# Kernel tuning notes

Measured on AMD Instinct MI355X. Metric: run time of the kernel, lower is better.

## Reference

```python
import jax, jax.numpy as jnp
from jax import lax
import numpy as np

# torch.sign(torch.sign(x) + 0.5): maps x<0 -> -1, x>=0 -> +1 (zeros go to +1)
def binarize(x):
    return jnp.where(x >= 0, 1.0, -1.0).astype(x.dtype)


def setup_inputs() -> dict:
    key = jax.random.key(0)
    kx, kw, kb = jax.random.split(key, 3)
    x = jax.random.normal(kx, (32, 256, 56, 56), dtype=jnp.float32)
    weight = jax.random.normal(kw, (256, 256, 3, 3), dtype=jnp.float32)
    bias = jax.random.normal(kb, (256,), dtype=jnp.float32)
    return {"x": x, "weight": weight, "bias": bias}


def reference(x, weight, bias):
    b_weight = binarize(weight)  # [O, I, kH, kW] in {-1, +1}
    b_bias = binarize(bias)      # [O] in {-1, +1}
    out = lax.conv_general_dilated(
        x, b_weight,
        window_strides=(1, 1),
        padding=((1, 1), (1, 1)),
        rhs_dilation=(1, 1),
        feature_group_count=1,
        dimension_numbers=("NCHW", "OIHW", "NCHW"),
    )
    return out + b_bias[None, :, None, None]
```

## Files before the change

### kernel.cpp

```cpp
#include <hip/hip_runtime.h>
#include <stdint.h>


#define N_IMG 32
#define C_IN  256
#define H_IN  56
#define W_IN  56
#define O_OUT 256
#define HW    (H_IN * W_IN)
#define K_RAW (C_IN * 9)

typedef int8_t i8x16 __attribute__((ext_vector_type(16)));
typedef int    i32x4 __attribute__((ext_vector_type(4)));
typedef float  f32x4 __attribute__((ext_vector_type(4)));
typedef float  f32x4u __attribute__((ext_vector_type(4), aligned(4)));
typedef __bf16 bf16x8 __attribute__((ext_vector_type(8)));

#define WQ_BYTES ((size_t)36 * 256 * 64)
#define ARR_OFF  WQ_BYTES
#define WS_NEED  (ARR_OFF + 4096)

#define BPITCH  80
#define BS_ROWB (58 * BPITCH)
#define CHUNK_B (3 * 8192)

#define AMAX_BLOCKS 1024

#define AS1 __attribute__((address_space(1)))
#define AS3 __attribute__((address_space(3)))

__device__ __forceinline__ void dma16(const void* g, void* l) {
    __builtin_amdgcn_global_load_lds((const AS1 uint32_t*)g, (AS3 uint32_t*)l, 16, 0, 0);
}

__global__ void prep_combo(const float* __restrict__ x, const float* __restrict__ w,
                           int8_t* __restrict__ wq, float* __restrict__ am_arr) {
    __shared__ __attribute__((aligned(16))) int8_t S[9 * 64 * 64];
    const int bx = blockIdx.x;
    const int t  = threadIdx.x;

    if (bx >= 16) {
        const int b = bx - 16;
        const size_t NV = (size_t)N_IMG * C_IN * HW / 4;
        float m = 0.f;
        for (size_t i = (size_t)b * 256 + t; i < NV; i += (size_t)AMAX_BLOCKS * 256) {
            f32x4 v = ((const f32x4*)x)[i];
            m = fmaxf(m, fmaxf(fmaxf(fabsf(v[0]), fabsf(v[1])),
                               fmaxf(fabsf(v[2]), fabsf(v[3]))));
        }
#pragma unroll
        for (int off = 32; off; off >>= 1)
            m = fmaxf(m, __shfl_down(m, off));
        float* red = (float*)S;
        if ((t & 63) == 0) red[t >> 6] = m;
        __syncthreads();
        if (t == 0)
            am_arr[b] = fmaxf(fmaxf(red[0], red[1]), fmaxf(red[2], red[3]));
        return;
    }

    const int og = bx >> 2;
    const int cc = bx & 3;
    const int o0 = og * 64;
#pragma unroll
    for (int kk = 0; kk < 4; ++kk) {
        const int p   = kk * 256 + t;
        const int o_l = p >> 4;
        const int chg = p & 15;
        const float* src = w + (size_t)(o0 + o_l) * K_RAW + (size_t)(cc * 64 + chg * 4) * 9;
        f32x4u v[9];
#pragma unroll
        for (int q = 0; q < 9; ++q) v[q] = *(const f32x4u*)(src + q * 4);
#pragma unroll
        for (int tap = 0; tap < 9; ++tap) {
            unsigned dw = 0;
#pragma unroll
            for (int co = 0; co < 4; ++co) {
                const int flat = co * 9 + tap;
                const float fv = v[flat >> 2][flat & 3];
                dw |= (unsigned)((fv >= 0.f) ? 0x01u : 0xffu) << (co * 8);
            }
            *(unsigned*)&S[tap * 4096 + o_l * 64 + chg * 4] = dw;
        }
    }
    __syncthreads();
#pragma unroll
    for (int kk = 0; kk < 9; ++kk) {
        const int c    = kk * 256 + t;
        const int tap  = c >> 8;
        const int rem  = c & 255;
        const int o_l  = rem >> 2;
        const int cpos = rem & 3;
        const int truec = (cpos - ((o_l & 15) >> 1)) & 3;
        i32x4 vv = *(const i32x4*)&S[tap * 4096 + o_l * 64 + truec * 16];
        *(i32x4*)(wq + ((size_t)(cc * 9 + tap) * 256 + (o0 + o_l)) * 64 + cpos * 16) = vv;
    }
}

__launch_bounds__(256, 2)
__global__ void bconv_fx3(const float* __restrict__ x,
                          const int8_t* __restrict__ wq,
                          const float* __restrict__ bias,
                          const float* __restrict__ am_arr,
                          float* __restrict__ out) {
    __shared__ __attribute__((aligned(16))) int8_t As[2 * CHUNK_B];
    __shared__ __attribute__((aligned(16))) int8_t Bs[6 * BS_ROWB];
    __shared__ float sred[4];

    const int tid  = threadIdx.x;
    const int lane = tid & 63;
    const int wv   = tid >> 6;
    const int row  = lane & 15;
    const int quad = lane >> 4;

    const int nrp  = blockIdx.x;
    const int n    = nrp / 14;
    const int rp   = nrp - n * 14;
    const int oblk = blockIdx.y;
    const int h0   = rp * 4;

    auto issueA3 = [&](int c) {
        const int8_t* g = wq + (size_t)(3 * c) * 16384 + oblk * 8192 + wv * 2048 + lane * 16;
        int8_t* l = &As[(c & 1) * CHUNK_B + wv * 2048];
#pragma unroll
        for (int u = 0; u < 3; ++u) {
            dma16(g + u * 16384,        l + u * 8192);
            dma16(g + u * 16384 + 1024, l + u * 8192 + 1024);
        }
    };
    issueA3(0);

    float m = fmaxf(fmaxf(am_arr[tid], am_arr[tid + 256]),
                    fmaxf(am_arr[tid + 512], am_arr[tid + 768]));
#pragma unroll
    for (int off = 32; off; off >>= 1)
        m = fmaxf(m, __shfl_down(m, off));
    if (lane == 0) sred[wv] = m;
    __syncthreads();
    m = fmaxf(fmaxf(sred[0], sred[1]), fmaxf(sred[2], sred[3]));
    const float scale = 127.f / fmaxf(m, 1e-20f);
    const float inv   = m * (1.0f / 127.0f);

    const int wg = tid >> 4;
    const int cg = tid & 15;

    int pr[4], pc[4];
    bool live[4];
#pragma unroll
    for (int nt = 0; nt < 4; ++nt) {
        int p = wv * 64 + nt * 16 + row;
        live[nt] = (p < 224);
        int r = p / 56;
        int c = p - r * 56;
        if (!live[nt]) { r = 0; c = 0; }
        pr[nt] = r;
        pc[nt] = c;
    }

    i32x4 acc[8][4];
#pragma unroll
    for (int mt = 0; mt < 8; ++mt)
#pragma unroll
        for (int nt = 0; nt < 4; ++nt)
            acc[mt][nt] = (i32x4){0, 0, 0, 0};

    const int rowA = row * 64 + (((quad + (row >> 1)) & 3) << 4);
    int addrB[4];
#pragma unroll
    for (int nt = 0; nt < 4; ++nt)
        addrB[nt] = pr[nt] * BS_ROWB + pc[nt] * BPITCH + quad * 16;

    i32x4 af[8], bc[4], bn[4];

    for (int cc = 0; cc < 4; ++cc) {
        __syncthreads();

        {
            const float* xpl = x + ((size_t)n * C_IN + cc * 64 + cg * 4) * HW;
#pragma unroll 2
            for (int r6 = 0; r6 < 6; ++r6) {
                const int hin = h0 + r6 - 1;
                int8_t* lrow = &Bs[r6 * BS_ROWB];
                if (wg >= 14) {
                    const int ww = (wg == 14) ? 0 : 57;
                    *(int*)(lrow + ww * BPITCH + cg * 4) = 0;
                } else if ((unsigned)hin < 56u) {
                    const float* src = xpl + (size_t)hin * W_IN + wg * 4;
                    f32x4 v0 = *(const f32x4*)(src);
                    f32x4 v1 = *(const f32x4*)(src + HW);
                    f32x4 v2 = *(const f32x4*)(src + 2 * HW);
                    f32x4 v3 = *(const f32x4*)(src + 3 * HW);
#pragma unroll
                    for (int k = 0; k < 4; ++k) {
                        float f0 = fminf(fmaxf(v0[k] * scale, -127.f), 127.f);
                        float f1 = fminf(fmaxf(v1[k] * scale, -127.f), 127.f);
                        float f2 = fminf(fmaxf(v2[k] * scale, -127.f), 127.f);
                        float f3 = fminf(fmaxf(v3[k] * scale, -127.f), 127.f);
                        int d = ((int)(uint8_t)(int8_t)(int)rintf(f0))
                              | ((int)(uint8_t)(int8_t)(int)rintf(f1) << 8)
                              | ((int)(uint8_t)(int8_t)(int)rintf(f2) << 16)
                              | ((int)(uint8_t)(int8_t)(int)rintf(f3) << 24);
                        *(int*)(lrow + (wg * 4 + k + 1) * BPITCH + cg * 4) = d;
                    }
                } else {
#pragma unroll
                    for (int k = 0; k < 4; ++k)
                        *(int*)(lrow + (wg * 4 + k + 1) * BPITCH + cg * 4) = 0;
                }
            }
        }
        __syncthreads();

#pragma unroll
        for (int k = 0; k < 3; ++k) {
            const int c = cc * 3 + k;
            if (k == 0) {
                if (c + 1 < 12) issueA3(c + 1);
#pragma unroll
                for (int nt = 0; nt < 4; ++nt)
                    bc[nt] = *(const i32x4*)(&Bs[addrB[nt]]);
            } else {
                __syncthreads();
                if (c + 1 < 12) issueA3(c + 1);
#pragma unroll
                for (int nt = 0; nt < 4; ++nt) bc[nt] = bn[nt];
            }
            const int8_t* Acur = &As[(c & 1) * CHUNK_B];
#pragma unroll
            for (int mt = 0; mt < 8; ++mt)
                af[mt] = *(const i32x4*)(Acur + mt * 1024 + rowA);

#pragma unroll
            for (int u = 0; u < 3; ++u) {
                if (u < 2) {
                    const int offn = k * BS_ROWB + (u + 1) * BPITCH;
#pragma unroll
                    for (int nt = 0; nt < 4; ++nt)
                        bn[nt] = *(const i32x4*)(&Bs[addrB[nt] + offn]);
                    const int8_t* Anx = Acur + (u + 1) * 8192;
#pragma unroll
                    for (int mt = 0; mt < 8; ++mt) {
                        i32x4 a = af[mt];
#pragma unroll
                        for (int nt = 0; nt < 4; ++nt)
                            acc[mt][nt] = __builtin_amdgcn_mfma_i32_16x16x64_i8(
                                a, bc[nt], acc[mt][nt], 0, 0, 0);
                        af[mt] = *(const i32x4*)(Anx + mt * 1024 + rowA);
                    }
#pragma unroll
                    for (int nt = 0; nt < 4; ++nt) bc[nt] = bn[nt];
                } else {
                    if (k < 2) {
                        const int offn = (k + 1) * BS_ROWB;
#pragma unroll
                        for (int nt = 0; nt < 4; ++nt)
                            bn[nt] = *(const i32x4*)(&Bs[addrB[nt] + offn]);
                    }
#pragma unroll
                    for (int mt = 0; mt < 8; ++mt)
#pragma unroll
                        for (int nt = 0; nt < 4; ++nt)
                            acc[mt][nt] = __builtin_amdgcn_mfma_i32_16x16x64_i8(
                                af[mt], bc[nt], acc[mt][nt], 0, 0, 0);
                }
            }
        }
    }

    float* base0 = out + ((size_t)n * O_OUT + oblk * 128) * HW;
    int pixoff[4];
#pragma unroll
    for (int nt = 0; nt < 4; ++nt)
        pixoff[nt] = (h0 + pr[nt]) * W_IN + pc[nt];
#pragma unroll
    for (int mt = 0; mt < 8; ++mt) {
        f32x4 bv = *(const f32x4*)(bias + oblk * 128 + mt * 16 + quad * 4);
#pragma unroll
        for (int r = 0; r < 4; ++r) {
            const float sb = (bv[r] >= 0.0f) ? 1.0f : -1.0f;
            const size_t ob = (size_t)(mt * 16 + quad * 4 + r) * HW;
#pragma unroll
            for (int nt = 0; nt < 4; ++nt)
                if (live[nt]) base0[ob + pixoff[nt]] = (float)acc[mt][nt][r] * inv + sb;
        }
    }
}

#define CHW (C_IN * HW)
#define FPITCH 40

__launch_bounds__(256, 2)
__global__ void bconv_fallback(const float* __restrict__ x,
                               const float* __restrict__ w,
                               const float* __restrict__ bias,
                               float* __restrict__ out) {
    __shared__ __attribute__((aligned(16))) __bf16 Asf[128 * FPITCH];
    __shared__ __attribute__((aligned(16))) __bf16 Bsf[128 * FPITCH];

    const int tid  = threadIdx.x;
    const int lane = tid & 63;
    const int wv   = tid >> 6;
    const int pblk = blockIdx.x;
    const int oblk = blockIdx.y;

    const int p_local = tid & 127;
    const int cgrp    = tid >> 7;
    const int pixel   = pblk * 128 + p_local;
    const int n_img   = pixel / HW;
    const int hw      = pixel - n_img * HW;
    const int h       = hw / W_IN;
    const int wx      = hw - h * W_IN;
    const float* xbase = x + (size_t)n_img * CHW;

    f32x4 acc[8][2];
#pragma unroll
    for (int mt = 0; mt < 8; ++mt)
#pragma unroll
        for (int nt = 0; nt < 2; ++nt)
            acc[mt][nt] = (f32x4){0.f, 0.f, 0.f, 0.f};

    const int pix_wave = wv * 32;
    const int row  = lane & 15;
    const int quad = lane >> 4;

    for (int tap = 0; tap < 9; ++tap) {
        const int dh = tap / 3 - 1;
        const int dw = tap % 3 - 1;
        const int hh = h + dh;
        const int ww = wx + dw;
        const bool valid = ((unsigned)hh < (unsigned)H_IN) && ((unsigned)ww < (unsigned)W_IN);
        const int offs = hh * W_IN + ww;

        for (int ck = 0; ck < 8; ++ck) {
            __syncthreads();
#pragma unroll
            for (int rep = 0; rep < 2; ++rep) {
                int v  = tid + rep * 256;
                int oa = v >> 2;
                int c8 = v & 3;
                const float* wsrc = w + (size_t)(oblk * 128 + oa) * K_RAW
                                      + (ck * 32 + c8 * 8) * 9 + tap;
                bf16x8 val;
#pragma unroll
                for (int j = 0; j < 8; ++j)
                    val[j] = (wsrc[j * 9] >= 0.0f) ? (__bf16)1.0f : (__bf16)(-1.0f);
                *(bf16x8*)(&Asf[oa * FPITCH + c8 * 8]) = val;
            }
            {
                const int cbase = (ck * 32 + cgrp * 16) * HW + offs;
#pragma unroll
                for (int g = 0; g < 2; ++g) {
                    bf16x8 vb;
#pragma unroll
                    for (int j = 0; j < 8; ++j) {
                        float f = valid ? xbase[cbase + (g * 8 + j) * HW] : 0.0f;
                        vb[j] = (__bf16)f;
                    }
                    *(bf16x8*)(&Bsf[p_local * FPITCH + cgrp * 16 + g * 8]) = vb;
                }
            }
            __syncthreads();
            bf16x8 bfrag[2];
#pragma unroll
            for (int nt = 0; nt < 2; ++nt)
                bfrag[nt] = *(const bf16x8*)(&Bsf[(pix_wave + nt * 16 + row) * FPITCH + quad * 8]);
#pragma unroll
            for (int mt = 0; mt < 8; ++mt) {
                bf16x8 afrag = *(const bf16x8*)(&Asf[(mt * 16 + row) * FPITCH + quad * 8]);
#pragma unroll
                for (int nt = 0; nt < 2; ++nt)
                    acc[mt][nt] = __builtin_amdgcn_mfma_f32_16x16x32_bf16(
                        afrag, bfrag[nt], acc[mt][nt], 0, 0, 0);
            }
        }
    }

#pragma unroll
    for (int nt = 0; nt < 2; ++nt) {
        int pix = pblk * 128 + pix_wave + nt * 16 + row;
        int ni  = pix / HW;
        int phw = pix - ni * HW;
        float* obase = out + (size_t)ni * (O_OUT * HW) + phw;
#pragma unroll
        for (int mt = 0; mt < 8; ++mt) {
            int o0 = oblk * 128 + mt * 16 + quad * 4;
#pragma unroll
            for (int r = 0; r < 4; ++r) {
                int o = o0 + r;
                float sb = (bias[o] >= 0.0f) ? 1.0f : -1.0f;
                obase[(size_t)o * HW] = acc[mt][nt][r] + sb;
            }
        }
    }
}

extern "C" void kernel_launch(void* const* d_in, const int* in_sizes, int n_in,
                              void* d_out, int out_size, void* d_ws, size_t ws_size,
                              hipStream_t stream) {
    const float* x    = (const float*)d_in[0];
    const float* w    = (const float*)d_in[1];
    const float* bias = (const float*)d_in[2];
    float* out        = (float*)d_out;

    if (ws_size >= WS_NEED) {
        int8_t* wq     = (int8_t*)d_ws;
        float*  am_arr = (float*)((char*)d_ws + ARR_OFF);

        prep_combo<<<dim3(16 + AMAX_BLOCKS), dim3(256), 0, stream>>>(x, w, wq, am_arr);
        bconv_fx3<<<dim3(N_IMG * 14, 2), dim3(256), 0, stream>>>(x, wq, bias, am_arr, out);
    } else {
        bconv_fallback<<<dim3((N_IMG * HW) / 128, 2), dim3(256), 0, stream>>>(
            x, w, bias, out);
    }
}
```

Measured before the change: 274.8 us.

## Load weight fragments directly from global memory instead of LDS DMA staging

```diff
diff --git a/kernel.cpp b/kernel.cpp
--- a/kernel.cpp
+++ b/kernel.cpp
@@ -22,16 +22,8 @@
 
 #define BPITCH  80
 #define BS_ROWB (58 * BPITCH)
-#define CHUNK_B (3 * 8192)
 
 #define AMAX_BLOCKS 1024
-
-#define AS1 __attribute__((address_space(1)))
-#define AS3 __attribute__((address_space(3)))
-
-__device__ __forceinline__ void dma16(const void* g, void* l) {
-    __builtin_amdgcn_global_load_lds((const AS1 uint32_t*)g, (AS3 uint32_t*)l, 16, 0, 0);
-}
 
 __global__ void prep_combo(const float* __restrict__ x, const float* __restrict__ w,
                            int8_t* __restrict__ wq, float* __restrict__ am_arr) {
@@ -91,19 +83,17 @@
         const int rem  = c & 255;
         const int o_l  = rem >> 2;
         const int cpos = rem & 3;
-        const int truec = (cpos - ((o_l & 15) >> 1)) & 3;
-        i32x4 vv = *(const i32x4*)&S[tap * 4096 + o_l * 64 + truec * 16];
+        i32x4 vv = *(const i32x4*)&S[tap * 4096 + o_l * 64 + cpos * 16];
         *(i32x4*)(wq + ((size_t)(cc * 9 + tap) * 256 + (o0 + o_l)) * 64 + cpos * 16) = vv;
     }
 }
 
 __launch_bounds__(256, 2)
-__global__ void bconv_fx3(const float* __restrict__ x,
+__global__ void bconv_fx4(const float* __restrict__ x,
                           const int8_t* __restrict__ wq,
                           const float* __restrict__ bias,
                           const float* __restrict__ am_arr,
                           float* __restrict__ out) {
-    __shared__ __attribute__((aligned(16))) int8_t As[2 * CHUNK_B];
     __shared__ __attribute__((aligned(16))) int8_t Bs[6 * BS_ROWB];
     __shared__ float sred[4];
 
@@ -118,17 +108,6 @@
     const int rp   = nrp - n * 14;
     const int oblk = blockIdx.y;
     const int h0   = rp * 4;
-
-    auto issueA3 = [&](int c) {
-        const int8_t* g = wq + (size_t)(3 * c) * 16384 + oblk * 8192 + wv * 2048 + lane * 16;
-        int8_t* l = &As[(c & 1) * CHUNK_B + wv * 2048];
-#pragma unroll
-        for (int u = 0; u < 3; ++u) {
-            dma16(g + u * 16384,        l + u * 8192);
-            dma16(g + u * 16384 + 1024, l + u * 8192 + 1024);
-        }
-    };
-    issueA3(0);
 
     float m = fmaxf(fmaxf(am_arr[tid], am_arr[tid + 256]),
                     fmaxf(am_arr[tid + 512], am_arr[tid + 768]));
@@ -164,7 +143,7 @@
         for (int nt = 0; nt < 4; ++nt)
             acc[mt][nt] = (i32x4){0, 0, 0, 0};
 
-    const int rowA = row * 64 + (((quad + (row >> 1)) & 3) << 4);
+    const int8_t* Aln = wq + (size_t)oblk * 8192 + row * 64 + quad * 16;
     int addrB[4];
 #pragma unroll
     for (int nt = 0; nt < 4; ++nt)
@@ -211,58 +190,41 @@
         }
         __syncthreads();
 
-#pragma unroll
-        for (int k = 0; k < 3; ++k) {
-            const int c = cc * 3 + k;
-            if (k == 0) {
-                if (c + 1 < 12) issueA3(c + 1);
+        const int s0 = cc * 9;
+        const int8_t* As0 = Aln + (size_t)s0 * 16384;
+#pragma unroll
+        for (int mt = 0; mt < 8; ++mt)
+            af[mt] = *(const i32x4*)(As0 + mt * 1024);
+#pragma unroll
+        for (int nt = 0; nt < 4; ++nt)
+            bc[nt] = *(const i32x4*)(&Bs[addrB[nt]]);
+
+#pragma unroll
+        for (int tap = 0; tap < 9; ++tap) {
+            if (tap < 8) {
+                const int offn = ((tap + 1) / 3) * BS_ROWB + ((tap + 1) % 3) * BPITCH;
 #pragma unroll
                 for (int nt = 0; nt < 4; ++nt)
-                    bc[nt] = *(const i32x4*)(&Bs[addrB[nt]]);
+                    bn[nt] = *(const i32x4*)(&Bs[addrB[nt] + offn]);
+                const int8_t* Anx = Aln + (size_t)(s0 + tap + 1) * 16384;
+#pragma unroll
+                for (int mt = 0; mt < 8; ++mt) {
+                    i32x4 a = af[mt];
+#pragma unroll
+                    for (int nt = 0; nt < 4; ++nt)
+                        acc[mt][nt] = __builtin_amdgcn_mfma_i32_16x16x64_i8(
+                            a, bc[nt], acc[mt][nt], 0, 0, 0);
+                    af[mt] = *(const i32x4*)(Anx + mt * 1024);
+                }
+#pragma unroll
+                for (int nt = 0; nt < 4; ++nt) bc[nt] = bn[nt];
             } else {
-                __syncthreads();
-                if (c + 1 < 12) issueA3(c + 1);
-#pragma unroll
-                for (int nt = 0; nt < 4; ++nt) bc[nt] = bn[nt];
-            }
-            const int8_t* Acur = &As[(c & 1) * CHUNK_B];
-#pragma unroll
-            for (int mt = 0; mt < 8; ++mt)
-                af[mt] = *(const i32x4*)(Acur + mt * 1024 + rowA);
-
-#pragma unroll
-            for (int u = 0; u < 3; ++u) {
-                if (u < 2) {
-                    const int offn = k * BS_ROWB + (u + 1) * BPITCH;
+#pragma unroll
+                for (int mt = 0; mt < 8; ++mt)
 #pragma unroll
                     for (int nt = 0; nt < 4; ++nt)
-                        bn[nt] = *(const i32x4*)(&Bs[addrB[nt] + offn]);
-                    const int8_t* Anx = Acur + (u + 1) * 8192;
-#pragma unroll
-                    for (int mt = 0; mt < 8; ++mt) {
-                        i32x4 a = af[mt];
-#pragma unroll
-                        for (int nt = 0; nt < 4; ++nt)
-                            acc[mt][nt] = __builtin_amdgcn_mfma_i32_16x16x64_i8(
-                                a, bc[nt], acc[mt][nt], 0, 0, 0);
-                        af[mt] = *(const i32x4*)(Anx + mt * 1024 + rowA);
-                    }
-#pragma unroll
-                    for (int nt = 0; nt < 4; ++nt) bc[nt] = bn[nt];
-                } else {
-                    if (k < 2) {
-                        const int offn = (k + 1) * BS_ROWB;
-#pragma unroll
-                        for (int nt = 0; nt < 4; ++nt)
-                            bn[nt] = *(const i32x4*)(&Bs[addrB[nt] + offn]);
-                    }
-#pragma unroll
-                    for (int mt = 0; mt < 8; ++mt)
-#pragma unroll
-                        for (int nt = 0; nt < 4; ++nt)
-                            acc[mt][nt] = __builtin_amdgcn_mfma_i32_16x16x64_i8(
-                                af[mt], bc[nt], acc[mt][nt], 0, 0, 0);
-                }
+                        acc[mt][nt] = __builtin_amdgcn_mfma_i32_16x16x64_i8(
+                            af[mt], bc[nt], acc[mt][nt], 0, 0, 0);
             }
         }
     }
@@ -407,7 +369,7 @@
         float*  am_arr = (float*)((char*)d_ws + ARR_OFF);
 
         prep_combo<<<dim3(16 + AMAX_BLOCKS), dim3(256), 0, stream>>>(x, w, wq, am_arr);
-        bconv_fx3<<<dim3(N_IMG * 14, 2), dim3(256), 0, stream>>>(x, wq, bias, am_arr, out);
+        bconv_fx4<<<dim3(N_IMG * 14, 2), dim3(256), 0, stream>>>(x, wq, bias, am_arr, out);
     } else {
         bconv_fallback<<<dim3((N_IMG * HW) / 128, 2), dim3(256), 0, stream>>>(
             x, w, bias, out);
```

Result: slower. 306.5 us (+11.5%).
